# Kernel optimization log

Hardware: AMD Instinct MI355X
Metric: run time of the kernel (lower is better)

Reference implementation:

```python
import jax, jax.numpy as jnp
import numpy as np

B, SEQ, DIM = 2, 2048, 1024
HEADS, HEAD_DIM = 16, 64
HIDDEN = 2816
EPS = 1e-5
LN_EPS = 1e-5


def rmsnorm(x, w, eps=EPS):
    return x * jax.lax.rsqrt(jnp.mean(x * x, axis=-1, keepdims=True) + eps) * w


def layernorm(x, w, b, eps=LN_EPS):
    mu = jnp.mean(x, axis=-1, keepdims=True)
    var = jnp.mean((x - mu) ** 2, axis=-1, keepdims=True)
    return (x - mu) * jax.lax.rsqrt(var + eps) * w + b


def modulate(x, shift, scale):
    # x: [B,S,D], shift/scale: [B,D]
    return x * (1.0 + scale[:, None, :]) + shift[:, None, :]


def apply_rope(t, cos, sin):
    # t: [B,S,H,D]; cos/sin: [S, D/2] -> complex multiply on (even,odd) pairs
    t = t.reshape(*t.shape[:-1], HEAD_DIM // 2, 2)
    t0, t1 = t[..., 0], t[..., 1]
    c = cos[None, :, None, :]
    s = sin[None, :, None, :]
    o0 = t0 * c - t1 * s
    o1 = t0 * s + t1 * c
    return jnp.stack([o0, o1], axis=-1).reshape(*t.shape[:-2], HEAD_DIM)


def setup_inputs() -> dict:
    key = jax.random.key(0)
    ks = jax.random.split(key, 12)
    def w(k, shape, s=0.02):
        return jax.random.normal(k, shape, dtype=jnp.float32) * s
    x = jax.random.normal(ks[0], (B, SEQ, DIM), dtype=jnp.float32)
    adaln_input = jax.random.normal(ks[1], (B, DIM), dtype=jnp.float32)
    pos = jnp.arange(SEQ, dtype=jnp.float32)
    inv_freq = 1.0 / (10000.0 ** (jnp.arange(0, HEAD_DIM, 2, dtype=jnp.float32) / HEAD_DIM))
    ang = pos[:, None] * inv_freq[None, :]  # [S, D/2]
    return dict(
        x=x, adaln_input=adaln_input,
        freqs_cos=jnp.cos(ang), freqs_sin=jnp.sin(ang),
        wq=w(ks[2], (DIM, DIM)), wk=w(ks[3], (DIM, DIM)),
        wv=w(ks[4], (DIM, DIM)), wo=w(ks[5], (DIM, DIM)),
        q_norm_w=jnp.ones(DIM, jnp.float32), q_norm_b=jnp.zeros(DIM, jnp.float32),
        k_norm_w=jnp.ones(DIM, jnp.float32), k_norm_b=jnp.zeros(DIM, jnp.float32),
        attn_norm_w=jnp.ones(DIM, jnp.float32), ffn_norm_w=jnp.ones(DIM, jnp.float32),
        ada_w=w(ks[6], (DIM, 6 * DIM)), ada_b=jnp.zeros(6 * DIM, jnp.float32),
        w1=w(ks[7], (DIM, HIDDEN)), w2=w(ks[8], (HIDDEN, DIM)), w3=w(ks[9], (DIM, HIDDEN)),
    )


def reference(x, adaln_input, freqs_cos, freqs_sin, wq, wk, wv, wo,
              q_norm_w, q_norm_b, k_norm_w, k_norm_b,
              attn_norm_w, ffn_norm_w, ada_w, ada_b, w1, w2, w3):
    # adaLN modulation: SiLU -> Linear -> 6 chunks of [B, DIM]
    m = jax.nn.silu(adaln_input) @ ada_w + ada_b
    shift_msa, scale_msa, gate_msa, shift_mlp, scale_mlp, gate_mlp = jnp.split(m, 6, axis=1)

    # --- attention branch ---
    h = modulate(rmsnorm(x, attn_norm_w), shift_msa, scale_msa)
    xq = layernorm(h @ wq, q_norm_w, q_norm_b)
    xk = layernorm(h @ wk, k_norm_w, k_norm_b)
    xv = h @ wv
    xq = xq.reshape(B, SEQ, HEADS, HEAD_DIM)
    xk = xk.reshape(B, SEQ, HEADS, HEAD_DIM)
    xv = xv.reshape(B, SEQ, HEADS, HEAD_DIM)
    xq = apply_rope(xq, freqs_cos, freqs_sin)
    xk = apply_rope(xk, freqs_cos, freqs_sin)
    scale = 1.0 / jnp.sqrt(jnp.float32(HEAD_DIM))
    scores = jnp.einsum('bshd,bthd->bhst', xq, xk) * scale  # [B,H,S,S]
    probs = jax.nn.softmax(scores, axis=-1)
    attn = jnp.einsum('bhst,bthd->bshd', probs, xv).reshape(B, SEQ, DIM)
    attn = attn @ wo
    x = x + gate_msa[:, None, :] * attn

    # --- MLP branch (SwiGLU) ---
    h = modulate(rmsnorm(x, ffn_norm_w), shift_mlp, scale_mlp)
    ffn = (jax.nn.silu(h @ w1) * (h @ w3)) @ w2
    x = x + gate_mlp[:, None, :] * ffn
    return x
```

## Files before the change

kernel.cpp:

```cpp
#include <hip/hip_runtime.h>
#include <hip/hip_bf16.h>

#define B_   2
#define S_   2048
#define D_   1024
#define H_   16
#define HD_  64
#define HID_ 2816

typedef unsigned short u16;
typedef unsigned int   u32;
typedef __attribute__((ext_vector_type(8))) short short8;
typedef __attribute__((ext_vector_type(4))) float f32x4;

static __device__ __forceinline__ float bf2f(u16 u){ return __uint_as_float(((u32)u)<<16); }
static __device__ __forceinline__ u16 f2bf(float f){
  u32 u = __float_as_uint(f);
  u32 r = (u + 0x7FFFu + ((u>>16)&1u)) >> 16;
  return (u16)r;
}

static __device__ __forceinline__ void ld4(const u16* p, float* v){
  ushort4 t = *reinterpret_cast<const ushort4*>(p);
  v[0]=bf2f(t.x); v[1]=bf2f(t.y); v[2]=bf2f(t.z); v[3]=bf2f(t.w);
}
static __device__ __forceinline__ void ld4(const float* p, float* v){
  float4 t = *reinterpret_cast<const float4*>(p);
  v[0]=t.x; v[1]=t.y; v[2]=t.z; v[3]=t.w;
}
static __device__ __forceinline__ void st4(u16* p, const float* v){
  ushort4 t; t.x=f2bf(v[0]); t.y=f2bf(v[1]); t.z=f2bf(v[2]); t.w=f2bf(v[3]);
  *reinterpret_cast<ushort4*>(p)=t;
}

static __device__ __forceinline__ float ld1g(const void* p, size_t i, bool f32){
  return f32 ? ((const float*)p)[i] : bf2f(((const u16*)p)[i]);
}
static __device__ __forceinline__ void ld4g(const void* p, size_t i, float* v, bool f32){
  if(f32){
    float4 t = *reinterpret_cast<const float4*>((const float*)p + i);
    v[0]=t.x; v[1]=t.y; v[2]=t.z; v[3]=t.w;
  }else{
    ushort4 t = *reinterpret_cast<const ushort4*>((const u16*)p + i);
    v[0]=bf2f(t.x); v[1]=bf2f(t.y); v[2]=bf2f(t.z); v[3]=bf2f(t.w);
  }
}
static __device__ __forceinline__ void st4g(void* p, size_t i, const float* v, bool f32){
  if(f32){
    float4 t; t.x=v[0]; t.y=v[1]; t.z=v[2]; t.w=v[3];
    *reinterpret_cast<float4*>((float*)p + i) = t;
  }else{
    st4((u16*)p + i, v);
  }
}

static __device__ __forceinline__ void gl2lds16(const u16* g, const u16* l){
  typedef __attribute__((address_space(3))) u16 lds_u16;
  typedef const __attribute__((address_space(1))) u16 glb_u16;
  __builtin_amdgcn_global_load_lds((glb_u16*)(uintptr_t)g,
                                   (lds_u16*)(u32)(uintptr_t)l, 16, 0, 0);
}

__global__ void k_probe(const u16* fc_raw, int* flag){
  if(threadIdx.x==0 && blockIdx.x==0) *flag = (fc_raw[0]==0) ? 1 : 0;
}

__global__ __launch_bounds__(256) void k_zero(float* p, int n){
  int i = blockIdx.x*256 + threadIdx.x;
  if(i<n) p[i] = 0.f;
}

static __device__ __forceinline__ float blk_sum(float v, float* red){
  #pragma unroll
  for(int o=32;o;o>>=1) v += __shfl_xor(v,o,64);
  int lane = threadIdx.x & 63, w = threadIdx.x >> 6;
  if(lane==0) red[w]=v;
  __syncthreads();
  float t = red[0]+red[1]+red[2]+red[3];
  __syncthreads();
  return t;
}

__global__ __launch_bounds__(256) void k_adaln(const void* a, const void* W, const void* bias,
                                               float* m, const int* flag){
  bool f32 = flag[0] != 0;
  __shared__ float sl[2][128];
  int bk = blockIdx.y;
  {
    int bb = threadIdx.x >> 7, kk = threadIdx.x & 127;
    float x = ld1g(a, bb*D_ + bk*128 + kk, f32);
    sl[bb][kk] = x/(1.f+__expf(-x));
  }
  __syncthreads();
  int n = blockIdx.x*256 + threadIdx.x;
  float p0 = 0.f, p1 = 0.f;
  for(int kk=0;kk<128;kk++){
    float w = ld1g(W, (size_t)(bk*128+kk)*6144 + n, f32);
    p0 += sl[0][kk]*w; p1 += sl[1][kk]*w;
  }
  if(bk==0){ float bv = ld1g(bias, n, f32); p0 += bv; p1 += bv; }
  atomicAdd(&m[n], p0);
  atomicAdd(&m[6144+n], p1);
}

__global__ __launch_bounds__(256) void k_rms_mod(const void* x, const void* nw, const float* m,
                                                 u16* h, int shift_off, int scale_off,
                                                 const int* flag, int force_f32x){
  bool f32in = flag[0] != 0;
  bool f32x  = force_f32x ? true : f32in;
  __shared__ float red[4];
  int row = blockIdx.x; int b = row >> 11;
  int d0 = threadIdx.x*4;
  float v[4]; ld4g(x, (size_t)row*D_ + d0, v, f32x);
  float ss = v[0]*v[0]+v[1]*v[1]+v[2]*v[2]+v[3]*v[3];
  float tot = blk_sum(ss, red);
  float r = rsqrtf(tot*(1.f/D_) + 1e-5f);
  const float* mb = m + b*6144;
  float wn[4]; ld4g(nw, d0, wn, f32in);
  float o[4];
  #pragma unroll
  for(int j=0;j<4;j++){
    int d = d0+j;
    o[j] = v[j]*r*wn[j]*(1.f+mb[scale_off+d]) + mb[shift_off+d];
  }
  st4(h + (size_t)row*D_ + d0, o);
}

__global__ __launch_bounds__(256) void k_ln_rope(u16* t, int str, const void* w, const void* bb,
                                                 const void* fc, const void* fs, const int* flag){
  bool f32 = flag[0] != 0;
  __shared__ float red[4];
  int row = blockIdx.x; int s = row & (S_-1);
  int d0 = threadIdx.x*4;
  u16* tp = t + (size_t)row*str + d0;
  float v[4]; ld4(tp, v);
  float sm = v[0]+v[1]+v[2]+v[3];
  float sq = v[0]*v[0]+v[1]*v[1]+v[2]*v[2]+v[3]*v[3];
  float tsm = blk_sum(sm, red);
  float tsq = blk_sum(sq, red);
  float mu  = tsm*(1.f/D_);
  float var = tsq*(1.f/D_) - mu*mu;
  float rs  = rsqrtf(var + 1e-5f);
  float wv[4], bv[4]; ld4g(w, d0, wv, f32); ld4g(bb, d0, bv, f32);
  float y[4];
  #pragma unroll
  for(int j=0;j<4;j++) y[j] = (v[j]-mu)*rs*wv[j] + bv[j];
  int pos = d0 & 63; int i0 = pos>>1;
  float c0 = ld1g(fc, s*32+i0,   f32), s0 = ld1g(fs, s*32+i0,   f32);
  float c1 = ld1g(fc, s*32+i0+1, f32), s1 = ld1g(fs, s*32+i0+1, f32);
  float o[4];
  o[0] = y[0]*c0 - y[1]*s0;
  o[1] = y[0]*s0 + y[1]*c0;
  o[2] = y[2]*c1 - y[3]*s1;
  o[3] = y[2]*s1 + y[3]*c1;
  st4(tp, o);
}

__global__ __launch_bounds__(256) void k_wt(const void* W, u16* WT, int Kd, int Nd,
                                            const int* flag){
  bool f32 = flag[0] != 0;
  __shared__ u16 L[64][72];
  int tid = threadIdx.x;
  int k0 = blockIdx.x*64, n0 = blockIdx.y*64;
  int r = tid>>2, c0 = (tid&3)*16;
  if(f32){
    const float* Wf = (const float*)W;
    #pragma unroll
    for(int j=0;j<4;j++){
      float4 t = *reinterpret_cast<const float4*>(&Wf[(size_t)(k0+r)*Nd + n0 + c0 + j*4]);
      L[r][c0+j*4+0]=f2bf(t.x); L[r][c0+j*4+1]=f2bf(t.y);
      L[r][c0+j*4+2]=f2bf(t.z); L[r][c0+j*4+3]=f2bf(t.w);
    }
  }else{
    const u16* Wh = (const u16*)W;
    *reinterpret_cast<short8*>(&L[r][c0]) =
      *reinterpret_cast<const short8*>(&Wh[(size_t)(k0+r)*Nd + n0 + c0]);
    *reinterpret_cast<short8*>(&L[r][c0+8]) =
      *reinterpret_cast<const short8*>(&Wh[(size_t)(k0+r)*Nd + n0 + c0 + 8]);
  }
  __syncthreads();
  int n = tid>>2, kk0 = (tid&3)*16;
  u16 tmp[16];
  #pragma unroll
  for(int j=0;j<16;j++) tmp[j] = L[kk0+j][n];
  u16* dst = WT + (size_t)(n0+n)*Kd + k0 + kk0;
  *reinterpret_cast<short8*>(dst)   = *reinterpret_cast<const short8*>(tmp);
  *reinterpret_cast<short8*>(dst+8) = *reinterpret_cast<const short8*>(tmp+8);
}

template<int TM>
__global__ __launch_bounds__(256) void k_gemm_mfma(const u16* A, int lda, const u16* BT, int ldb,
                                                   u16* C, int M, int N, int K){
  __shared__ __align__(16) u16 As[TM*64];
  __shared__ __align__(16) u16 Bs[128*64];
  int tid = threadIdx.x, lane = tid&63, w = tid>>6;
  int col = lane&15, quad = lane>>4;
  int row0 = blockIdx.y*TM, col0 = blockIdx.x*128;
  const u16* Ab = A  + (size_t)row0*lda;
  const u16* Bb = BT + (size_t)col0*ldb;
  constexpr int MI = TM/32;
  int wm = (w>>1)*(TM/2);
  int wn = (w&1)*64;
  f32x4 acc[MI][4];
  #pragma unroll
  for(int i=0;i<MI;i++)
    #pragma unroll
    for(int j=0;j<4;j++) acc[i][j] = (f32x4){0.f,0.f,0.f,0.f};

  for(int k0=0;k0<K;k0+=64){
    __syncthreads();
    #pragma unroll
    for(int i=0;i<TM/32;i++){
      int c = i*256 + w*64 + lane;
      int r = c>>3, s = c&7, gs = s ^ (r&7);
      gl2lds16(Ab + (size_t)r*lda + k0 + gs*8, As + (size_t)c*8);
    }
    #pragma unroll
    for(int i=0;i<4;i++){
      int c = i*256 + w*64 + lane;
      int r = c>>3, s = c&7, gs = s ^ (r&7);
      gl2lds16(Bb + (size_t)r*ldb + k0 + gs*8, Bs + (size_t)c*8);
    }
    __syncthreads();
    #pragma unroll
    for(int ks=0;ks<64;ks+=32){
      short8 af[MI], bfr[4];
      #pragma unroll
      for(int mi=0;mi<MI;mi++){
        int r = wm+mi*16+col;
        int sch = ((ks>>3) + quad) ^ (col&7);
        af[mi] = *reinterpret_cast<const short8*>(&As[r*64 + sch*8]);
      }
      #pragma unroll
      for(int ni=0;ni<4;ni++){
        int r = wn+ni*16+col;
        int sch = ((ks>>3) + quad) ^ (col&7);
        bfr[ni] = *reinterpret_cast<const short8*>(&Bs[r*64 + sch*8]);
      }
      #pragma unroll
      for(int mi=0;mi<MI;mi++)
        #pragma unroll
        for(int ni=0;ni<4;ni++)
          acc[mi][ni] = __builtin_amdgcn_mfma_f32_16x16x32_bf16(af[mi], bfr[ni], acc[mi][ni], 0,0,0);
    }
  }
  #pragma unroll
  for(int mi=0;mi<MI;mi++)
    #pragma unroll
    for(int r=0;r<4;r++){
      size_t rowoff = (size_t)(row0+wm+mi*16+quad*4+r)*N + col0 + wn;
      #pragma unroll
      for(int ni=0;ni<4;ni++)
        C[rowoff + ni*16 + col] = f2bf(acc[mi][ni][r]);
    }
}

__global__ __launch_bounds__(256) void k_vt(const u16* v, int vstr, u16* vt){
  __shared__ u16 L[64][72];
  int tid = threadIdx.x;
  int wg = blockIdx.x;
  int kblk = wg & 31; int bh = wg >> 5; int h = bh & 15, b = bh >> 4;
  int row = tid>>2, c0 = (tid&3)*16;
  const u16* src = v + (size_t)(b*S_ + kblk*64 + row)*vstr + h*HD_ + c0;
  *reinterpret_cast<short8*>(&L[row][c0])   = *reinterpret_cast<const short8*>(src);
  *reinterpret_cast<short8*>(&L[row][c0+8]) = *reinterpret_cast<const short8*>(src+8);
  __syncthreads();
  int hd = tid>>2, k0 = (tid&3)*16;
  u16 tmp[16];
  #pragma unroll
  for(int j=0;j<16;j++) tmp[j] = L[k0+j][hd];
  u16* dst = vt + ((size_t)bh*HD_ + hd)*S_ + kblk*64 + k0;
  *reinterpret_cast<short8*>(dst)   = *reinterpret_cast<const short8*>(tmp);
  *reinterpret_cast<short8*>(dst+8) = *reinterpret_cast<const short8*>(tmp+8);
}

__global__ __launch_bounds__(256) void k_attn_mfma(const u16* q, const u16* k, const u16* vt,
                                                   u16* o, int qks){
  __shared__ __align__(16) u16 Ks[64*88];
  __shared__ __align__(16) u16 Vs[64*88];
  int tid = threadIdx.x, lane = tid & 63, wid = tid >> 6;
  int col = lane & 15, quad = lane >> 4;
  int wg = blockIdx.x;
  int qblk = wg & 31; int bh = wg >> 5; int h = bh & 15, b = bh >> 4;

  const u16* kb  = k  + (size_t)b*S_*qks + h*HD_;
  const u16* vtb = vt + (size_t)bh*HD_*S_;

  short8 qa0, qa1;
  {
    const u16* qp = q + (size_t)(b*S_ + qblk*64 + wid*16 + col)*qks + h*HD_ + quad*8;
    short8 t0 = *reinterpret_cast<const short8*>(qp);
    short8 t1 = *reinterpret_cast<const short8*>(qp + 32);
    #pragma unroll
    for(int j=0;j<8;j++){
      qa0[j] = (short)f2bf(bf2f((u16)t0[j])*0.125f);
      qa1[j] = (short)f2bf(bf2f((u16)t1[j])*0.125f);
    }
  }
  float m_i = -1e30f, l_i = 0.f;
  f32x4 acc[4];
  #pragma unroll
  for(int t=0;t<4;t++) acc[t] = (f32x4){0.f,0.f,0.f,0.f};

  for(int t0=0;t0<S_;t0+=64){
    __syncthreads();
    #pragma unroll
    for(int g=0;g<2;g++){
      int c = g*256 + tid;
      int l = c>>3, kc = (c&7)*8;
      int kl = 32*(l>>5) + 8*((l>>2)&3) + 4*((l>>4)&1) + (l&3);
      *reinterpret_cast<short8*>(&Ks[l*88 + kc]) =
        *reinterpret_cast<const short8*>(kb + (size_t)(t0+kl)*qks + kc);
      *reinterpret_cast<short8*>(&Vs[l*88 + kc]) =
        *reinterpret_cast<const short8*>(vtb + (size_t)l*S_ + t0 + kc);
    }
    __syncthreads();

    f32x4 st[4];
    #pragma unroll
    for(int mt=0;mt<4;mt++){
      st[mt] = (f32x4){0.f,0.f,0.f,0.f};
      short8 ka0 = *reinterpret_cast<const short8*>(&Ks[(mt*16+col)*88 + quad*8]);
      short8 ka1 = *reinterpret_cast<const short8*>(&Ks[(mt*16+col)*88 + 32 + quad*8]);
      st[mt] = __builtin_amdgcn_mfma_f32_16x16x32_bf16(ka0, qa0, st[mt], 0,0,0);
      st[mt] = __builtin_amdgcn_mfma_f32_16x16x32_bf16(ka1, qa1, st[mt], 0,0,0);
    }
    float cm = st[0][0];
    #pragma unroll
    for(int mt=0;mt<4;mt++)
      #pragma unroll
      for(int r=0;r<4;r++) cm = fmaxf(cm, st[mt][r]);
    cm = fmaxf(cm, __shfl_xor(cm,16,64));
    cm = fmaxf(cm, __shfl_xor(cm,32,64));
    float mn = fmaxf(m_i, cm);
    float al = __expf(m_i - mn);
    float pe[4][4]; float ps = 0.f;
    #pragma unroll
    for(int mt=0;mt<4;mt++)
      #pragma unroll
      for(int r=0;r<4;r++){ pe[mt][r] = __expf(st[mt][r]-mn); ps += pe[mt][r]; }
    ps += __shfl_xor(ps,16,64);
    ps += __shfl_xor(ps,32,64);
    l_i = l_i*al + ps;
    m_i = mn;
    #pragma unroll
    for(int t=0;t<4;t++) acc[t] *= al;
    #pragma unroll
    for(int w=0;w<2;w++){
      short8 pb;
      #pragma unroll
      for(int p=0;p<8;p++) pb[p] = (short)f2bf(pe[2*w + (p>>2)][p&3]);
      #pragma unroll
      for(int ht=0;ht<4;ht++){
        short8 vf = *reinterpret_cast<const short8*>(&Vs[(ht*16+col)*88 + w*32 + quad*8]);
        acc[ht] = __builtin_amdgcn_mfma_f32_16x16x32_bf16(vf, pb, acc[ht], 0,0,0);
      }
    }
  }
  float inv = 1.f/l_i;
  u16* ob = o + (size_t)(b*S_ + qblk*64 + wid*16 + col)*D_ + h*HD_;
  #pragma unroll
  for(int ht=0;ht<4;ht++){
    ushort4 t;
    t.x = f2bf(acc[ht][0]*inv); t.y = f2bf(acc[ht][1]*inv);
    t.z = f2bf(acc[ht][2]*inv); t.w = f2bf(acc[ht][3]*inv);
    *reinterpret_cast<ushort4*>(ob + ht*16 + quad*4) = t;
  }
}

__global__ __launch_bounds__(256) void k_resid_f(const void* x, const u16* y, const float* m,
                                                 int gate_off, float* o, const int* flag){
  bool f32 = flag[0] != 0;
  size_t i4 = ((size_t)blockIdx.x*256 + threadIdx.x)*4;
  int d = (int)(i4 & (D_-1));
  int b = (int)(i4 >> 21);
  float xv[4], yv[4];
  ld4g(x, i4, xv, f32); ld4(y+i4, yv);
  const float* g = m + b*6144 + gate_off + d;
  float4 r; r.x=xv[0]+g[0]*yv[0]; r.y=xv[1]+g[1]*yv[1]; r.z=xv[2]+g[2]*yv[2]; r.w=xv[3]+g[3]*yv[3];
  *reinterpret_cast<float4*>(o+i4) = r;
}

__global__ __launch_bounds__(256) void k_resid_b(const float* x, const u16* y, const float* m,
                                                 int gate_off, void* o, const int* flag){
  bool f32 = flag[0] != 0;
  size_t i4 = ((size_t)blockIdx.x*256 + threadIdx.x)*4;
  int d = (int)(i4 & (D_-1));
  int b = (int)(i4 >> 21);
  float xv[4], yv[4];
  ld4(x+i4, xv); ld4(y+i4, yv);
  const float* g = m + b*6144 + gate_off + d;
  float r[4];
  #pragma unroll
  for(int j=0;j<4;j++) r[j] = xv[j] + g[j]*yv[j];
  st4g(o, i4, r, f32);
}

__global__ __launch_bounds__(256) void k_silu_mul(u16* h13){
  int c4 = (blockIdx.x*256 + threadIdx.x)*4;
  if(c4 >= HID_) return;
  u16* p = h13 + (size_t)blockIdx.y*5632 + c4;
  float a[4], c[4];
  ld4(p, a); ld4(p + HID_, c);
  float r[4];
  #pragma unroll
  for(int j=0;j<4;j++){ float sv = a[j]/(1.f+__expf(-a[j])); r[j] = sv*c[j]; }
  st4(p, r);
}

extern "C" void kernel_launch(void* const* d_in, const int* in_sizes, int n_in,
                              void* d_out, int out_size, void* d_ws, size_t ws_size,
                              hipStream_t stream){
  const void* x   = d_in[0];
  const void* ada = d_in[1];
  const void* fc  = d_in[2];
  const void* fs  = d_in[3];
  const void* wq  = d_in[4];
  const void* wk  = d_in[5];
  const void* wv  = d_in[6];
  const void* wo  = d_in[7];
  const void* qnw = d_in[8];
  const void* qnb = d_in[9];
  const void* knw = d_in[10];
  const void* knb = d_in[11];
  const void* anw = d_in[12];
  const void* fnw = d_in[13];
  const void* aw  = d_in[14];
  const void* ab  = d_in[15];
  const void* w1  = d_in[16];
  const void* w2  = d_in[17];
  const void* w3  = d_in[18];
  char* ws = (char*)d_ws;
  const size_t MB = 1u<<20;

  int*   flag = (int*)ws;
  float* m    = (float*)(ws + 4096);
  u16*  hbuf  = (u16*)(ws + 1*MB);
  u16*  xqkv  = (u16*)(ws + 9*MB);
  float* x2   = (float*)(ws + 9*MB);
  u16*  proj  = (u16*)(ws + 25*MB);
  u16*  wreg  = (u16*)(ws + 33*MB);
  u16*  h13   = (u16*)(ws + 45*MB);
  u16*  vt    = wreg;

  dim3 blk(256);

  k_probe<<<dim3(1), dim3(64), 0, stream>>>((const u16*)fc, flag);
  k_zero<<<dim3(48), blk, 0, stream>>>(m, 12288);
  k_adaln<<<dim3(24,8), blk, 0, stream>>>(ada, aw, ab, m, flag);
  k_rms_mod<<<dim3(B_*S_), blk, 0, stream>>>(x, anw, m, hbuf, 0, 1024, flag, 0);

  k_wt<<<dim3(16,16), blk, 0, stream>>>(wq, wreg,                1024, 1024, flag);
  k_wt<<<dim3(16,16), blk, 0, stream>>>(wk, wreg + 1024*1024,    1024, 1024, flag);
  k_wt<<<dim3(16,16), blk, 0, stream>>>(wv, wreg + 2*1024*1024,  1024, 1024, flag);
  k_gemm_mfma<128><<<dim3(24,32), blk, 0, stream>>>(hbuf, 1024, wreg, 1024, xqkv, 4096, 3072, 1024);

  k_ln_rope<<<dim3(B_*S_), blk, 0, stream>>>(xqkv,        3072, qnw, qnb, fc, fs, flag);
  k_ln_rope<<<dim3(B_*S_), blk, 0, stream>>>(xqkv + 1024, 3072, knw, knb, fc, fs, flag);
  k_vt<<<dim3(B_*H_*S_/64), blk, 0, stream>>>(xqkv + 2048, 3072, vt);
  k_attn_mfma<<<dim3(B_*H_*S_/64), blk, 0, stream>>>(xqkv, xqkv + 1024, vt, hbuf, 3072);

  k_wt<<<dim3(16,16), blk, 0, stream>>>(wo, wreg, 1024, 1024, flag);
  k_gemm_mfma<64><<<dim3(8,64), blk, 0, stream>>>(hbuf, 1024, wreg, 1024, proj, 4096, 1024, 1024);
  k_resid_f<<<dim3(4096), blk, 0, stream>>>(x, proj, m, 2048, x2, flag);
  k_rms_mod<<<dim3(B_*S_), blk, 0, stream>>>(x2, fnw, m, hbuf, 3072, 4096, flag, 1);

  k_wt<<<dim3(16,44), blk, 0, stream>>>(w1, wreg,               1024, 2816, flag);
  k_wt<<<dim3(16,44), blk, 0, stream>>>(w3, wreg + 2816*1024,   1024, 2816, flag);
  k_gemm_mfma<128><<<dim3(44,32), blk, 0, stream>>>(hbuf, 1024, wreg, 1024, h13, 4096, 5632, 1024);
  k_silu_mul<<<dim3(3,4096), blk, 0, stream>>>(h13);
  k_wt<<<dim3(44,16), blk, 0, stream>>>(w2, wreg, 2816, 1024, flag);
  k_gemm_mfma<64><<<dim3(8,64), blk, 0, stream>>>(h13, 5632, wreg, 2816, proj, 4096, 1024, 2816);
  k_resid_b<<<dim3(4096), blk, 0, stream>>>(x2, proj, m, 5120, d_out, flag);
}
```

Before: 466.6 us.

## Fuse small kernels, batch weight transposes, use exp2 softmax and cheaper bf16 packing

Merges the probe and zero kernels, combines the post-attention residual with the second RMSNorm, batches the weight transposes and the Q/K layernorm+rope launches through grid dimensions, and moves the attention softmax to exp2 by folding log2(e) into the Q scale. It also switches to round-half-up bf16 packing in the GEMM epilogue, transposes and attention, and hoists K/V load address math out of the attention loop. The aim is fewer launches, less memory traffic and fewer ALU ops in the attention inner loop. Rounding behaviour changes slightly, since ties are no longer rounded to even.

```diff
diff --git a/kernel.cpp b/kernel.cpp
--- a/kernel.cpp
+++ b/kernel.cpp
@@ -12,12 +12,19 @@
 typedef unsigned int   u32;
 typedef __attribute__((ext_vector_type(8))) short short8;
 typedef __attribute__((ext_vector_type(4))) float f32x4;
+typedef __attribute__((ext_vector_type(4))) u32   u32x4;
 
 static __device__ __forceinline__ float bf2f(u16 u){ return __uint_as_float(((u32)u)<<16); }
 static __device__ __forceinline__ u16 f2bf(float f){
   u32 u = __float_as_uint(f);
   u32 r = (u + 0x7FFFu + ((u>>16)&1u)) >> 16;
   return (u16)r;
+}
+static __device__ __forceinline__ u16 f2bfr(float f){
+  return (u16)((__float_as_uint(f) + 0x8000u) >> 16);
+}
+static __device__ __forceinline__ u32 pk2(float a, float b){
+  return ((__float_as_uint(a) + 0x8000u) >> 16) | ((__float_as_uint(b) + 0x8000u) & 0xFFFF0000u);
 }
 
 static __device__ __forceinline__ void ld4(const u16* p, float* v){
@@ -61,13 +68,10 @@
                                    (lds_u16*)(u32)(uintptr_t)l, 16, 0, 0);
 }
 
-__global__ void k_probe(const u16* fc_raw, int* flag){
-  if(threadIdx.x==0 && blockIdx.x==0) *flag = (fc_raw[0]==0) ? 1 : 0;
-}
-
-__global__ __launch_bounds__(256) void k_zero(float* p, int n){
+__global__ __launch_bounds__(256) void k_probe_zero(const u16* fc_raw, int* flag, float* m){
   int i = blockIdx.x*256 + threadIdx.x;
-  if(i<n) p[i] = 0.f;
+  if(i < 12288) m[i] = 0.f;
+  if(i == 0) *flag = (fc_raw[0]==0) ? 1 : 0;
 }
 
 static __device__ __forceinline__ float blk_sum(float v, float* red){
@@ -105,18 +109,17 @@
 
 __global__ __launch_bounds__(256) void k_rms_mod(const void* x, const void* nw, const float* m,
                                                  u16* h, int shift_off, int scale_off,
-                                                 const int* flag, int force_f32x){
-  bool f32in = flag[0] != 0;
-  bool f32x  = force_f32x ? true : f32in;
+                                                 const int* flag){
+  bool f32 = flag[0] != 0;
   __shared__ float red[4];
   int row = blockIdx.x; int b = row >> 11;
   int d0 = threadIdx.x*4;
-  float v[4]; ld4g(x, (size_t)row*D_ + d0, v, f32x);
+  float v[4]; ld4g(x, (size_t)row*D_ + d0, v, f32);
   float ss = v[0]*v[0]+v[1]*v[1]+v[2]*v[2]+v[3]*v[3];
   float tot = blk_sum(ss, red);
   float r = rsqrtf(tot*(1.f/D_) + 1e-5f);
   const float* mb = m + b*6144;
-  float wn[4]; ld4g(nw, d0, wn, f32in);
+  float wn[4]; ld4g(nw, d0, wn, f32);
   float o[4];
   #pragma unroll
   for(int j=0;j<4;j++){
@@ -126,13 +129,43 @@
   st4(h + (size_t)row*D_ + d0, o);
 }
 
-__global__ __launch_bounds__(256) void k_ln_rope(u16* t, int str, const void* w, const void* bb,
-                                                 const void* fc, const void* fs, const int* flag){
+__global__ __launch_bounds__(256) void k_resid_rms(const void* x, const u16* y, const float* m,
+                                                   const void* nw, float* x2, u16* h,
+                                                   const int* flag){
+  bool f32 = flag[0] != 0;
+  __shared__ float red[4];
+  int row = blockIdx.x; int b = row >> 11;
+  int d0 = threadIdx.x*4;
+  size_t i4 = (size_t)row*D_ + d0;
+  float xv[4], yv[4];
+  ld4g(x, i4, xv, f32); ld4(y+i4, yv);
+  const float* mb = m + b*6144;
+  float v[4];
+  #pragma unroll
+  for(int j=0;j<4;j++) v[j] = xv[j] + mb[2048+d0+j]*yv[j];
+  float4 t; t.x=v[0]; t.y=v[1]; t.z=v[2]; t.w=v[3];
+  *reinterpret_cast<float4*>(x2+i4) = t;
+  float ss = v[0]*v[0]+v[1]*v[1]+v[2]*v[2]+v[3]*v[3];
+  float tot = blk_sum(ss, red);
+  float r = rsqrtf(tot*(1.f/D_) + 1e-5f);
+  float wn[4]; ld4g(nw, d0, wn, f32);
+  float o[4];
+  #pragma unroll
+  for(int j=0;j<4;j++)
+    o[j] = v[j]*r*wn[j]*(1.f+mb[4096+d0+j]) + mb[3072+d0+j];
+  st4(h + i4, o);
+}
+
+__global__ __launch_bounds__(256) void k_ln_rope2(u16* t, const void* qw, const void* qb,
+                                                  const void* kw, const void* kb2,
+                                                  const void* fc, const void* fs, const int* flag){
   bool f32 = flag[0] != 0;
   __shared__ float red[4];
   int row = blockIdx.x; int s = row & (S_-1);
+  const void* w  = blockIdx.y ? kw  : qw;
+  const void* bb = blockIdx.y ? kb2 : qb;
   int d0 = threadIdx.x*4;
-  u16* tp = t + (size_t)row*str + d0;
+  u16* tp = t + (size_t)row*3072 + blockIdx.y*1024 + d0;
   float v[4]; ld4(tp, v);
   float sm = v[0]+v[1]+v[2]+v[3];
   float sq = v[0]*v[0]+v[1]*v[1]+v[2]*v[2]+v[3]*v[3];
@@ -156,9 +189,11 @@
   st4(tp, o);
 }
 
-__global__ __launch_bounds__(256) void k_wt(const void* W, u16* WT, int Kd, int Nd,
-                                            const int* flag){
+__global__ __launch_bounds__(256) void k_wt3(const void* W0, const void* W1, const void* W2,
+                                             u16* WT, int Kd, int Nd, const int* flag){
   bool f32 = flag[0] != 0;
+  const void* W = blockIdx.z==0 ? W0 : (blockIdx.z==1 ? W1 : W2);
+  u16* dst_base = WT + (size_t)blockIdx.z * (size_t)Kd * Nd;
   __shared__ u16 L[64][72];
   int tid = threadIdx.x;
   int k0 = blockIdx.x*64, n0 = blockIdx.y*64;
@@ -168,8 +203,8 @@
     #pragma unroll
     for(int j=0;j<4;j++){
       float4 t = *reinterpret_cast<const float4*>(&Wf[(size_t)(k0+r)*Nd + n0 + c0 + j*4]);
-      L[r][c0+j*4+0]=f2bf(t.x); L[r][c0+j*4+1]=f2bf(t.y);
-      L[r][c0+j*4+2]=f2bf(t.z); L[r][c0+j*4+3]=f2bf(t.w);
+      L[r][c0+j*4+0]=f2bfr(t.x); L[r][c0+j*4+1]=f2bfr(t.y);
+      L[r][c0+j*4+2]=f2bfr(t.z); L[r][c0+j*4+3]=f2bfr(t.w);
     }
   }else{
     const u16* Wh = (const u16*)W;
@@ -183,7 +218,7 @@
   u16 tmp[16];
   #pragma unroll
   for(int j=0;j<16;j++) tmp[j] = L[kk0+j][n];
-  u16* dst = WT + (size_t)(n0+n)*Kd + k0 + kk0;
+  u16* dst = dst_base + (size_t)(n0+n)*Kd + k0 + kk0;
   *reinterpret_cast<short8*>(dst)   = *reinterpret_cast<const short8*>(tmp);
   *reinterpret_cast<short8*>(dst+8) = *reinterpret_cast<const short8*>(tmp+8);
 }
@@ -251,7 +286,7 @@
       size_t rowoff = (size_t)(row0+wm+mi*16+quad*4+r)*N + col0 + wn;
       #pragma unroll
       for(int ni=0;ni<4;ni++)
-        C[rowoff + ni*16 + col] = f2bf(acc[mi][ni][r]);
+        C[rowoff + ni*16 + col] = f2bfr(acc[mi][ni][r]);
     }
 }
 
@@ -288,13 +323,14 @@
 
   short8 qa0, qa1;
   {
+    const float qscale = 0.18033688f;
     const u16* qp = q + (size_t)(b*S_ + qblk*64 + wid*16 + col)*qks + h*HD_ + quad*8;
     short8 t0 = *reinterpret_cast<const short8*>(qp);
     short8 t1 = *reinterpret_cast<const short8*>(qp + 32);
     #pragma unroll
     for(int j=0;j<8;j++){
-      qa0[j] = (short)f2bf(bf2f((u16)t0[j])*0.125f);
-      qa1[j] = (short)f2bf(bf2f((u16)t1[j])*0.125f);
+      qa0[j] = (short)f2bf(bf2f((u16)t0[j])*qscale);
+      qa1[j] = (short)f2bf(bf2f((u16)t1[j])*qscale);
     }
   }
   float m_i = -1e30f, l_i = 0.f;
@@ -302,17 +338,26 @@
   #pragma unroll
   for(int t=0;t<4;t++) acc[t] = (f32x4){0.f,0.f,0.f,0.f};
 
+  const u16 *kp[2]; const u16 *vp[2]; u16 *ksd[2], *vsd[2];
+  #pragma unroll
+  for(int g=0;g<2;g++){
+    int c = g*256 + tid;
+    int l = c>>3, kc = (c&7)*8;
+    int kl = 32*(l>>5) + 8*((l>>2)&3) + 4*((l>>4)&1) + (l&3);
+    kp[g]  = kb + (size_t)kl*qks + kc;
+    vp[g]  = vtb + (size_t)l*S_ + kc;
+    ksd[g] = Ks + l*88 + kc;
+    vsd[g] = Vs + l*88 + kc;
+  }
+
   for(int t0=0;t0<S_;t0+=64){
     __syncthreads();
     #pragma unroll
     for(int g=0;g<2;g++){
-      int c = g*256 + tid;
-      int l = c>>3, kc = (c&7)*8;
-      int kl = 32*(l>>5) + 8*((l>>2)&3) + 4*((l>>4)&1) + (l&3);
-      *reinterpret_cast<short8*>(&Ks[l*88 + kc]) =
-        *reinterpret_cast<const short8*>(kb + (size_t)(t0+kl)*qks + kc);
-      *reinterpret_cast<short8*>(&Vs[l*88 + kc]) =
-        *reinterpret_cast<const short8*>(vtb + (size_t)l*S_ + t0 + kc);
+      *reinterpret_cast<short8*>(ksd[g]) =
+        *reinterpret_cast<const short8*>(kp[g] + (size_t)t0*qks);
+      *reinterpret_cast<short8*>(vsd[g]) =
+        *reinterpret_cast<const short8*>(vp[g] + t0);
     }
     __syncthreads();
 
@@ -333,52 +378,47 @@
     cm = fmaxf(cm, __shfl_xor(cm,16,64));
     cm = fmaxf(cm, __shfl_xor(cm,32,64));
     float mn = fmaxf(m_i, cm);
-    float al = __expf(m_i - mn);
-    float pe[4][4]; float ps = 0.f;
+    float al = __builtin_amdgcn_exp2f(m_i - mn);
+    m_i = mn;
+    float pe[4][4];
     #pragma unroll
     for(int mt=0;mt<4;mt++)
       #pragma unroll
-      for(int r=0;r<4;r++){ pe[mt][r] = __expf(st[mt][r]-mn); ps += pe[mt][r]; }
-    ps += __shfl_xor(ps,16,64);
-    ps += __shfl_xor(ps,32,64);
-    l_i = l_i*al + ps;
-    m_i = mn;
+      for(int r=0;r<4;r++) pe[mt][r] = __builtin_amdgcn_exp2f(st[mt][r]-mn);
     #pragma unroll
     for(int t=0;t<4;t++) acc[t] *= al;
     #pragma unroll
     for(int w=0;w<2;w++){
-      short8 pb;
-      #pragma unroll
-      for(int p=0;p<8;p++) pb[p] = (short)f2bf(pe[2*w + (p>>2)][p&3]);
+      u32x4 pw;
+      pw[0] = pk2(pe[2*w][0],   pe[2*w][1]);
+      pw[1] = pk2(pe[2*w][2],   pe[2*w][3]);
+      pw[2] = pk2(pe[2*w+1][0], pe[2*w+1][1]);
+      pw[3] = pk2(pe[2*w+1][2], pe[2*w+1][3]);
+      short8 pb = *reinterpret_cast<short8*>(&pw);
       #pragma unroll
       for(int ht=0;ht<4;ht++){
         short8 vf = *reinterpret_cast<const short8*>(&Vs[(ht*16+col)*88 + w*32 + quad*8]);
         acc[ht] = __builtin_amdgcn_mfma_f32_16x16x32_bf16(vf, pb, acc[ht], 0,0,0);
       }
     }
-  }
-  float inv = 1.f/l_i;
+    float ps = 0.f;
+    #pragma unroll
+    for(int mt=0;mt<4;mt++)
+      #pragma unroll
+      for(int r=0;r<4;r++) ps += pe[mt][r];
+    ps += __shfl_xor(ps,16,64);
+    ps += __shfl_xor(ps,32,64);
+    l_i = l_i*al + ps;
+  }
+  float inv = __builtin_amdgcn_rcpf(l_i);
   u16* ob = o + (size_t)(b*S_ + qblk*64 + wid*16 + col)*D_ + h*HD_;
   #pragma unroll
   for(int ht=0;ht<4;ht++){
-    ushort4 t;
-    t.x = f2bf(acc[ht][0]*inv); t.y = f2bf(acc[ht][1]*inv);
-    t.z = f2bf(acc[ht][2]*inv); t.w = f2bf(acc[ht][3]*inv);
-    *reinterpret_cast<ushort4*>(ob + ht*16 + quad*4) = t;
-  }
-}
-
-__global__ __launch_bounds__(256) void k_resid_f(const void* x, const u16* y, const float* m,
-                                                 int gate_off, float* o, const int* flag){
-  bool f32 = flag[0] != 0;
-  size_t i4 = ((size_t)blockIdx.x*256 + threadIdx.x)*4;
-  int d = (int)(i4 & (D_-1));
-  int b = (int)(i4 >> 21);
-  float xv[4], yv[4];
-  ld4g(x, i4, xv, f32); ld4(y+i4, yv);
-  const float* g = m + b*6144 + gate_off + d;
-  float4 r; r.x=xv[0]+g[0]*yv[0]; r.y=xv[1]+g[1]*yv[1]; r.z=xv[2]+g[2]*yv[2]; r.w=xv[3]+g[3]*yv[3];
-  *reinterpret_cast<float4*>(o+i4) = r;
+    uint2 t;
+    t.x = pk2(acc[ht][0]*inv, acc[ht][1]*inv);
+    t.y = pk2(acc[ht][2]*inv, acc[ht][3]*inv);
+    *reinterpret_cast<uint2*>(ob + ht*16 + quad*4) = t;
+  }
 }
 
 __global__ __launch_bounds__(256) void k_resid_b(const float* x, const u16* y, const float* m,
@@ -445,31 +485,25 @@
 
   dim3 blk(256);
 
-  k_probe<<<dim3(1), dim3(64), 0, stream>>>((const u16*)fc, flag);
-  k_zero<<<dim3(48), blk, 0, stream>>>(m, 12288);
+  k_probe_zero<<<dim3(48), blk, 0, stream>>>((const u16*)fc, flag, m);
   k_adaln<<<dim3(24,8), blk, 0, stream>>>(ada, aw, ab, m, flag);
-  k_rms_mod<<<dim3(B_*S_), blk, 0, stream>>>(x, anw, m, hbuf, 0, 1024, flag, 0);
-
-  k_wt<<<dim3(16,16), blk, 0, stream>>>(wq, wreg,                1024, 1024, flag);
-  k_wt<<<dim3(16,16), blk, 0, stream>>>(wk, wreg + 1024*1024,    1024, 1024, flag);
-  k_wt<<<dim3(16,16), blk, 0, stream>>>(wv, wreg + 2*1024*1024,  1024, 1024, flag);
+  k_rms_mod<<<dim3(B_*S_), blk, 0, stream>>>(x, anw, m, hbuf, 0, 1024, flag);
+
+  k_wt3<<<dim3(16,16,3), blk, 0, stream>>>(wq, wk, wv, wreg, 1024, 1024, flag);
   k_gemm_mfma<128><<<dim3(24,32), blk, 0, stream>>>(hbuf, 1024, wreg, 1024, xqkv, 4096, 3072, 1024);
 
-  k_ln_rope<<<dim3(B_*S_), blk, 0, stream>>>(xqkv,        3072, qnw, qnb, fc, fs, flag);
-  k_ln_rope<<<dim3(B_*S_), blk, 0, stream>>>(xqkv + 1024, 3072, knw, knb, fc, fs, flag);
+  k_ln_rope2<<<dim3(B_*S_,2), blk, 0, stream>>>(xqkv, qnw, qnb, knw, knb, fc, fs, flag);
   k_vt<<<dim3(B_*H_*S_/64), blk, 0, stream>>>(xqkv + 2048, 3072, vt);
   k_attn_mfma<<<dim3(B_*H_*S_/64), blk, 0, stream>>>(xqkv, xqkv + 1024, vt, hbuf, 3072);
 
-  k_wt<<<dim3(16,16), blk, 0, stream>>>(wo, wreg, 1024, 1024, flag);
+  k_wt3<<<dim3(16,16,1), blk, 0, stream>>>(wo, wo, wo, wreg, 1024, 1024, flag);
   k_gemm_mfma<64><<<dim3(8,64), blk, 0, stream>>>(hbuf, 1024, wreg, 1024, proj, 4096, 1024, 1024);
-  k_resid_f<<<dim3(4096), blk, 0, stream>>>(x, proj, m, 2048, x2, flag);
-  k_rms_mod<<<dim3(B_*S_), blk, 0, stream>>>(x2, fnw, m, hbuf, 3072, 4096, flag, 1);
-
-  k_wt<<<dim3(16,44), blk, 0, stream>>>(w1, wreg,               1024, 2816, flag);
-  k_wt<<<dim3(16,44), blk, 0, stream>>>(w3, wreg + 2816*1024,   1024, 2816, flag);
+  k_resid_rms<<<dim3(B_*S_), blk, 0, stream>>>(x, proj, m, fnw, x2, hbuf, flag);
+
+  k_wt3<<<dim3(16,44,2), blk, 0, stream>>>(w1, w3, w3, wreg, 1024, 2816, flag);
   k_gemm_mfma<128><<<dim3(44,32), blk, 0, stream>>>(hbuf, 1024, wreg, 1024, h13, 4096, 5632, 1024);
   k_silu_mul<<<dim3(3,4096), blk, 0, stream>>>(h13);
-  k_wt<<<dim3(44,16), blk, 0, stream>>>(w2, wreg, 2816, 1024, flag);
+  k_wt3<<<dim3(44,16,1), blk, 0, stream>>>(w2, w2, w2, wreg, 2816, 1024, flag);
   k_gemm_mfma<64><<<dim3(8,64), blk, 0, stream>>>(h13, 5632, wreg, 2816, proj, 4096, 1024, 2816);
   k_resid_b<<<dim3(4096), blk, 0, stream>>>(x2, proj, m, 5120, d_out, flag);
 }
```

After: 457.1 us. -2.0%, faster.
